# Optimization experiments

Hardware: AMD Instinct MI355X
Metric: run time of the kernel (lower is better)

## Reference

```python
import jax, jax.numpy as jnp
import numpy as np

# module constants (from init_kwargs)
CS, NV, ED = 8, 4, 32          # codebook_size, num_variables, embedding_dim
VIEWS, D, KSZ = 3, 16, 3        # num_input_channels, depth, kernel_size
HW = 14                         # 7 * scale (scale=2)
CSP = 8                         # spatial of conv_shape after three valid 3x3 convs: 14->12->10->8
KSTATES = CS ** NV              # 4096 combinatorial discrete states


def _elu(x):
    return jnp.where(x > 0, x, jnp.expm1(x))


def _conv_t(x, w, b):
    # PyTorch ConvTranspose2d(stride=1, padding=0); w: (Cin, Cout, k, k)
    wf = jnp.flip(w, (2, 3)).transpose(1, 0, 2, 3)  # -> (Cout, Cin, k, k)
    p = w.shape[2] - 1
    y = jax.lax.conv_general_dilated(x, wf, (1, 1), [(p, p), (p, p)],
                                     dimension_numbers=('NCHW', 'OIHW', 'NCHW'))
    return y + b[None, :, None, None]


def setup_inputs() -> dict:
    key = jax.random.key(0)
    ks = jax.random.split(key, 10)
    rn = lambda k, shape, s=1.0: jax.random.normal(k, shape, jnp.float32) * s
    return {
        'x': rn(ks[0], (64, VIEWS, HW, HW)),
        'latent_embedding': rn(ks[1], (NV, CS, ED)),
        'lin_w': rn(ks[2], (VIEWS, ED * NV, 4 * D * CSP * CSP), 0.05),
        'lin_b': rn(ks[3], (VIEWS, 4 * D * CSP * CSP), 0.05),
        'w1': rn(ks[4], (VIEWS, 4 * D, 2 * D, KSZ, KSZ), 0.05),
        'b1': rn(ks[5], (VIEWS, 2 * D), 0.05),
        'w2': rn(ks[6], (VIEWS, 2 * D, D, KSZ, KSZ), 0.05),
        'b2': rn(ks[7], (VIEWS, D), 0.05),
        'w3': rn(ks[8], (VIEWS, D, 1, KSZ, KSZ), 0.05),
        'b3': rn(ks[9], (VIEWS, 1), 0.05),
    }


def reference(x, latent_embedding, lin_w, lin_b, w1, b1, w2, b2, w3, b3):
    # all combinations of codebook indices (itertools.product order): [K, NV]
    all_idcs = jnp.stack(
        jnp.meshgrid(*([jnp.arange(CS)] * NV), indexing='ij'), -1).reshape(-1, NV)
    # gather: z[k, v, :] = latent_embedding[v, all_idcs[k, v], :]
    z = latent_embedding[jnp.arange(NV)[None, :], all_idcs]       # [K, NV, ED]
    zf = z.reshape(KSTATES, NV * ED)                              # 'b n d -> b (n d)'

    def decode(lw, lb, W1, B1, W2, B2, W3, B3):
        h = (zf @ lw + lb).reshape(KSTATES, 4 * D, CSP, CSP)
        h = _elu(_conv_t(h, W1, B1))
        h = _elu(_conv_t(h, W2, B2))
        h = _conv_t(h, W3, B3)
        return h[:, 0]                                            # [K, HW, HW]

    m = jax.vmap(decode)(lin_w, lin_b, w1, b1, w2, b2, w3, b3)    # [views, K, HW, HW]
    m = jnp.transpose(m, (1, 0, 2, 3))                            # [K, views, HW, HW]

    # obs_logits = -0.5 * sum_{h,w} (m[None] - x[:, None])**2, computed without
    # materializing the [B, K, views, HW, HW] broadcast tensor
    m2 = jnp.sum(m * m, axis=(-2, -1))                            # [K, views]
    x2 = jnp.sum(x * x, axis=(-2, -1))                            # [B, views]
    cross = jnp.einsum('kvhw,bvhw->bkv', m, x)                    # [B, K, views]
    return -0.5 * (m2[None] + x2[:, None] - 2.0 * cross)          # [B, K, views]
```

## Files before the change

### kernel.cpp

```cpp
#include <hip/hip_runtime.h>
#include <cstddef>


typedef __attribute__((ext_vector_type(4))) float f32x4;
typedef _Float16 half8v __attribute__((ext_vector_type(8)));
typedef _Float16 half4v __attribute__((ext_vector_type(4)));
typedef _Float16 half2v __attribute__((ext_vector_type(2)));

static __device__ __forceinline__ float elu(float s) {
    float e = __expf(s) - 1.0f;
    return s > 0.f ? s : e;
}
static __device__ __forceinline__ float dot2acc(int hpair, int wpair, float acc) {
#if __has_builtin(__builtin_amdgcn_fdot2)
    return __builtin_amdgcn_fdot2(__builtin_bit_cast(half2v, hpair),
                                  __builtin_bit_cast(half2v, wpair), acc, false);
#else
    half2v h = __builtin_bit_cast(half2v, hpair);
    half2v w = __builtin_bit_cast(half2v, wpair);
    acc = fmaf((float)h.x, (float)w.x, acc);
    return fmaf((float)h.y, (float)w.y, acc);
#endif
}
static __device__ __forceinline__ int sh2addr(int c, int r) {
    return c * 392 + r * 24 + (((r >> 2) & 3) << 3);
}

__global__ __launch_bounds__(320) void prep_kernel(const float* __restrict__ x,
                                                   const float* __restrict__ le,
                                                   const float* __restrict__ lin_w,
                                                   const float* __restrict__ lin_b,
                                                   const float* __restrict__ w1,
                                                   const float* __restrict__ b1,
                                                   const float* __restrict__ w2,
                                                   float* __restrict__ Qa,
                                                   float* __restrict__ Qb,
                                                   float* __restrict__ x2,
                                                   short* __restrict__ xB,
                                                   short* __restrict__ Wf) {
    int bid = blockIdx.x;
    int t = threadIdx.x;
    if (bid >= 198) {
        int pid = bid - 198;
        int v = pid % 3, part = pid / 3;
        if (part < 4) {
            int nb = part;
            short* xBv = xB + v * 14336 + nb * 3584;
            for (int idx = t; idx < 3584; idx += 320) {
                int j = idx & 7, lane = (idx >> 3) & 63, s = idx >> 9;
                int px = s * 32 + ((lane >> 4) << 3) + j;
                int b  = nb * 16 + (lane & 15);
                float val = (px < 196) ? x[(b * 3 + v) * 196 + px] : 0.f;
                _Float16 h = (_Float16)val;
                xBv[idx] = __builtin_bit_cast(short, h);
            }
        } else if (part == 4) {
            int w = t >> 6, lane = t & 63;
            for (int b = w; b < 64; b += 5) {
                const float* xp = x + (b * 3 + v) * 196;
                float s = 0.f;
                for (int px = lane; px < 196; px += 64) s = fmaf(xp[px], xp[px], s);
#pragma unroll
                for (int off = 32; off; off >>= 1) s += __shfl_down(s, off, 64);
                if (lane == 0) x2[v * 64 + b] = s;
            }
        } else if (t < 64) {
            int lane = t;
            const float* w2v = w2 + v * 32 * 16 * 9;
            int co = lane & 15;
            int cibase = (lane >> 4) * 8;
#pragma unroll
            for (int tap = 0; tap < 9; ++tap)
#pragma unroll
                for (int j = 0; j < 8; ++j) {
                    _Float16 h = (_Float16)w2v[((cibase + j) * 16 + co) * 9 + tap];
                    Wf[(((v * 9 + tap) * 64 + lane) << 3) + j] = __builtin_bit_cast(short, h);
                }
        }
        return;
    }
    __shared__ float sPt[64 * 144];
    __shared__ float sW[16 * 32 * 9];
    int row = bid % 33;
    int v   = (bid / 33) % 3;
    int z   = bid / 99;

    float pj[16];
    if (t < 256) {
        if (row < 32) {
            int vp = row >> 3;
            const float* base0 = lin_w + (size_t)v * 524288 + (size_t)vp * 131072 + t * 16;
            const float* lep = le + row * 32;
            f32x4 a0 = {0,0,0,0}, a1 = {0,0,0,0}, a2 = {0,0,0,0}, a3 = {0,0,0,0};
            for (int e = 0; e < 32; ++e) {
                float lv = lep[e];
                const float4* bp = (const float4*)(base0 + e * 4096);
                float4 b0 = bp[0], b1v_ = bp[1], b2v_ = bp[2], b3v_ = bp[3];
                a0[0] = fmaf(lv, b0.x, a0[0]);  a0[1] = fmaf(lv, b0.y, a0[1]);
                a0[2] = fmaf(lv, b0.z, a0[2]);  a0[3] = fmaf(lv, b0.w, a0[3]);
                a1[0] = fmaf(lv, b1v_.x, a1[0]); a1[1] = fmaf(lv, b1v_.y, a1[1]);
                a1[2] = fmaf(lv, b1v_.z, a1[2]); a1[3] = fmaf(lv, b1v_.w, a1[3]);
                a2[0] = fmaf(lv, b2v_.x, a2[0]); a2[1] = fmaf(lv, b2v_.y, a2[1]);
                a2[2] = fmaf(lv, b2v_.z, a2[2]); a2[3] = fmaf(lv, b2v_.w, a2[3]);
                a3[0] = fmaf(lv, b3v_.x, a3[0]); a3[1] = fmaf(lv, b3v_.y, a3[1]);
                a3[2] = fmaf(lv, b3v_.z, a3[2]); a3[3] = fmaf(lv, b3v_.w, a3[3]);
            }
#pragma unroll
            for (int j = 0; j < 4; ++j) {
                pj[j] = a0[j]; pj[4 + j] = a1[j]; pj[8 + j] = a2[j]; pj[12 + j] = a3[j];
            }
        } else {
            const float4* bp = (const float4*)(lin_b + v * 4096 + t * 16);
#pragma unroll
            for (int j = 0; j < 4; ++j) {
                float4 b = bp[j];
                pj[4 * j] = b.x; pj[4 * j + 1] = b.y; pj[4 * j + 2] = b.z; pj[4 * j + 3] = b.w;
            }
        }
    }
    float4* zp = (float4*)sPt;
    for (int i = t; i < 2304; i += 320) zp[i] = float4{0.f, 0.f, 0.f, 0.f};
    __syncthreads();
    if (t < 256) {
        int ci = t >> 2;
#pragma unroll
        for (int j = 0; j < 16; ++j) {
            int r = (t & 3) * 16 + j;
            int y = r >> 3, xx = r & 7;
            sPt[ci * 144 + (xx + 2) * 12 + (y + 2)] = pj[j];
        }
    }
    const float* w1v = w1 + (size_t)v * 18432;
    int co = t / 10, ox = t % 10;
    float acc[10];
#pragma unroll
    for (int i = 0; i < 10; ++i) acc[i] = 0.f;

    for (int c0 = z * 2; c0 < z * 2 + 2; ++c0) {
        __syncthreads();
        const float4* wsrc = (const float4*)(w1v + c0 * 4608);
        for (int i = t; i < 1152; i += 320) ((float4*)sW)[i] = wsrc[i];
        __syncthreads();
#pragma unroll 2
        for (int ci = 0; ci < 16; ++ci) {
            const float* xp = sPt + (c0 * 16 + ci) * 144;
            const float* wp = sW + (ci * 32 + co) * 9;
            float wv[9];
#pragma unroll
            for (int j = 0; j < 9; ++j) wv[j] = wp[j];
#pragma unroll
            for (int b = 0; b < 3; ++b) {
                const float* colp = xp + (ox + 2 - b) * 12;
                float4 c0v = *(const float4*)(colp);
                float4 c1v = *(const float4*)(colp + 4);
                float4 c2v = *(const float4*)(colp + 8);
                float cv[12] = {c0v.x, c0v.y, c0v.z, c0v.w,
                                c1v.x, c1v.y, c1v.z, c1v.w,
                                c2v.x, c2v.y, c2v.z, c2v.w};
#pragma unroll
                for (int a = 0; a < 3; ++a) {
                    float wgt = wv[a * 3 + b];
#pragma unroll
                    for (int oy = 0; oy < 10; ++oy)
                        acc[oy] = fmaf(cv[oy + 2 - a], wgt, acc[oy]);
                }
            }
        }
    }
    float bb = (z == 0 && row == 32) ? b1[v * 32 + co] : 0.f;
    float* dst = (z == 0 ? Qa : Qb) + (size_t)v * 105600 + row * 3200;
#pragma unroll
    for (int oy = 0; oy < 10; ++oy)
        dst[(ox * 10 + oy) * 32 + co] = acc[oy] + bb;
}

__global__ __launch_bounds__(256) void fusedgemm_kernel(const float* __restrict__ Qa,
                                                        const float* __restrict__ Qb,
                                                        const short* __restrict__ Wf,
                                                        const float* __restrict__ b2,
                                                        const float* __restrict__ w3,
                                                        const float* __restrict__ b3,
                                                        const short* __restrict__ xB,
                                                        const float* __restrict__ x2g,
                                                        float* __restrict__ out) {
    __shared__ alignas(16) short sH1[196 * 40];
    __shared__ alignas(16) short sH2[6280];
    __shared__ alignas(16) short sM[16 * 224];
    __shared__ alignas(16) float sQ[3200];
    __shared__ int sW3p[72];
    __shared__ float sM2[16];
    int k0 = blockIdx.x * 16;
    int v = blockIdx.y;
    int t = threadIdx.x;
    int lane = t & 63;
    int g = lane >> 4;
    int w = t >> 6;

    half8v bfrag[9];
#pragma unroll
    for (int tap = 0; tap < 9; ++tap)
        bfrag[tap] = *(const half8v*)(const void*)(Wf + (((v * 9 + tap) * 64 + lane) << 3));
    float bias2 = b2[v * 16 + (lane & 15)];
    float bias3 = b3[v];

    if (t < 16) sM2[t] = 0.f;
    for (int pix = t; pix < 196; pix += 256) {
        int c = pix / 14, r = pix % 14;
        if (c < 2 || c >= 12 || r < 2 || r >= 12) {
            int4* z = (int4*)(sH1 + pix * 40);
            z[0] = int4{0,0,0,0}; z[1] = int4{0,0,0,0};
            z[2] = int4{0,0,0,0}; z[3] = int4{0,0,0,0};
        }
    }
    {
        int c = t >> 4, r = t & 15;
        if (c < 2 || c >= 14 || r < 2 || r >= 14) {
            int4* z = (int4*)(sH2 + sh2addr(c, r));
            z[0] = int4{0,0,0,0}; z[1] = int4{0,0,0,0};
        }
    }
    if (t < 72) {
        int tap = t / 8, j = t % 8;
        half2v p = {(_Float16)w3[v * 144 + (2 * j) * 9 + tap],
                    (_Float16)w3[v * 144 + (2 * j + 1) * 9 + tap]};
        sW3p[t] = __builtin_bit_cast(int, p);
    }

    int st1[4]; bool v1[4];
    {
        int ci4 = (t & 7) * 4;
#pragma unroll
        for (int j = 0; j < 4; ++j) {
            int i = t + j * 256;
            v1[j] = (i < 800);
            int pix = i >> 3;
            int cx = pix / 10, ry = pix % 10;
            st1[j] = ((cx + 2) * 14 + (ry + 2)) * 40 + ci4;
        }
    }
    int ntile = 0; int bmoff[3]; int soff[3][4];
    for (int tile = w; tile < 9; tile += 4) {
        int m = tile * 16 + (lane & 15);
        int cx2 = m / 12, ry2 = m % 12;
        bmoff[ntile] = (cx2 * 14 + ry2) * 40 + g * 8;
        int p0 = tile * 16 + g * 4;
        int cxp = p0 / 12, ryp = p0 % 12;
        int co = lane & 15;
#pragma unroll
        for (int r = 0; r < 4; ++r) {
            soff[ntile][r] = sh2addr(cxp + 2, ryp + 2) + co;
            ++ryp; if (ryp == 12) { ryp = 0; ++cxp; }
        }
        ++ntile;
    }
    int off3[9];
    {
        int ry3 = (t < 196) ? t / 14 : 0;
        int cx3 = (t < 196) ? t % 14 : 0;
#pragma unroll
        for (int a = 0; a < 3; ++a)
#pragma unroll
            for (int b = 0; b < 3; ++b)
                off3[a * 3 + b] = sh2addr(cx3 + 2 - b, ry3 + 2 - a);
    }

    const float* Qav = Qa + (size_t)v * 105600;
    const float* Qbv = Qb + (size_t)v * 105600;
    int i0 = (k0 >> 9) & 7;
    int i1 = (k0 >> 6) & 7;
    int i2b = (k0 >> 3) & 7;

    for (int s = 0; s < 16; ++s) {
        if ((s & 7) == 0) {
            int i2 = i2b + (s >> 3);
            const float4* pa0 = (const float4*)(Qav + i0 * 3200);
            const float4* pb0 = (const float4*)(Qbv + i0 * 3200);
            const float4* pa1 = (const float4*)(Qav + (8 + i1) * 3200);
            const float4* pb1 = (const float4*)(Qbv + (8 + i1) * 3200);
            const float4* pa2 = (const float4*)(Qav + (16 + i2) * 3200);
            const float4* pb2 = (const float4*)(Qbv + (16 + i2) * 3200);
            const float4* pab = (const float4*)(Qav + 32 * 3200);
            const float4* pbb = (const float4*)(Qbv + 32 * 3200);
            float4* dq = (float4*)sQ;
            for (int i = t; i < 800; i += 256) {
                float4 A = pa0[i], B = pb0[i], C = pa1[i], D = pb1[i];
                float4 E = pa2[i], F = pb2[i], G = pab[i], H = pbb[i];
                dq[i] = float4{A.x + B.x + C.x + D.x + E.x + F.x + G.x + H.x,
                               A.y + B.y + C.y + D.y + E.y + F.y + G.y + H.y,
                               A.z + B.z + C.z + D.z + E.z + F.z + G.z + H.z,
                               A.w + B.w + C.w + D.w + E.w + F.w + G.w + H.w};
            }
            __syncthreads();
        }
        {
            int i3 = s & 7;
            const float4* qa3 = (const float4*)(Qav + (24 + i3) * 3200);
            const float4* qb3 = (const float4*)(Qbv + (24 + i3) * 3200);
            const float4* qs = (const float4*)sQ;
#pragma unroll
            for (int j = 0; j < 4; ++j) {
                if (v1[j]) {
                    int i = t + j * 256;
                    float4 q = qs[i], a = qa3[i], b = qb3[i];
                    half4v o = {(_Float16)elu(q.x + a.x + b.x),
                                (_Float16)elu(q.y + a.y + b.y),
                                (_Float16)elu(q.z + a.z + b.z),
                                (_Float16)elu(q.w + a.w + b.w)};
                    *(half4v*)(void*)(sH1 + st1[j]) = o;
                }
            }
        }
        __syncthreads();
#pragma unroll
        for (int it = 0; it < 3; ++it) {
            if (it < ntile) {
                const short* basemin = sH1 + bmoff[it];
                f32x4 acc0 = {bias2, bias2, bias2, bias2};
                f32x4 acc1 = {0.f, 0.f, 0.f, 0.f};
#pragma unroll
                for (int a = 0; a < 3; ++a)
#pragma unroll
                    for (int b = 0; b < 3; ++b) {
                        half8v af = *(const half8v*)(const void*)(basemin + ((2 - b) * 14 + (2 - a)) * 40);
                        int idx = a * 3 + b;
                        if (idx & 1)
                            acc1 = __builtin_amdgcn_mfma_f32_16x16x32_f16(af, bfrag[idx], acc1, 0, 0, 0);
                        else
                            acc0 = __builtin_amdgcn_mfma_f32_16x16x32_f16(af, bfrag[idx], acc0, 0, 0, 0);
                    }
#pragma unroll
                for (int r = 0; r < 4; ++r) {
                    _Float16 h = (_Float16)elu(acc0[r] + acc1[r]);
                    sH2[soff[it][r]] = __builtin_bit_cast(short, h);
                }
            }
        }
        __syncthreads();
        {
            float mval = 0.f;
            if (t < 196) {
                float a0 = bias3, a1 = 0.f, a2 = 0.f, a3 = 0.f;
#pragma unroll
                for (int tap = 0; tap < 9; ++tap) {
                    const short* base = sH2 + off3[tap];
                    int4 lo = *(const int4*)(const void*)(base);
                    int4 hi = *(const int4*)(const void*)(base + 8);
                    const int* wp = sW3p + tap * 8;
                    a0 = dot2acc(lo.x, wp[0], a0);
                    a1 = dot2acc(lo.y, wp[1], a1);
                    a2 = dot2acc(lo.z, wp[2], a2);
                    a3 = dot2acc(lo.w, wp[3], a3);
                    a0 = dot2acc(hi.x, wp[4], a0);
                    a1 = dot2acc(hi.y, wp[5], a1);
                    a2 = dot2acc(hi.z, wp[6], a2);
                    a3 = dot2acc(hi.w, wp[7], a3);
                }
                mval = (a0 + a1) + (a2 + a3);
            }
            if (t < 224) {
                _Float16 h = (_Float16)mval;
                sM[s * 224 + t] = __builtin_bit_cast(short, h);
            }
            float sq = mval * mval;
#pragma unroll
            for (int off = 32; off; off >>= 1) sq += __shfl_down(sq, off, 64);
            if (lane == 0) atomicAdd(&sM2[s], sq);
        }
    }
    __syncthreads();

    {
        f32x4 acc = {0.f, 0.f, 0.f, 0.f};
        const short* abase = sM + (lane & 15) * 224 + g * 8;
        const short* bbase = xB + (((v * 4 + w) * 7) * 64 + lane) * 8;
#pragma unroll
        for (int s7 = 0; s7 < 7; ++s7) {
            half8v af = *(const half8v*)(const void*)(abase + s7 * 32);
            half8v bf = *(const half8v*)(const void*)(bbase + s7 * 512);
            acc = __builtin_amdgcn_mfma_f32_16x16x32_f16(af, bf, acc, 0, 0, 0);
        }
        int b = w * 16 + (lane & 15);
        float x2v = x2g[v * 64 + b];
        size_t obase = ((size_t)b * 4096 + k0) * 3 + v;
#pragma unroll
        for (int r = 0; r < 4; ++r) {
            int kk = g * 4 + r;
            out[obase + (size_t)kk * 3] = acc[r] - 0.5f * (sM2[kk] + x2v);
        }
    }
}

extern "C" void kernel_launch(void* const* d_in, const int* in_sizes, int n_in,
                              void* d_out, int out_size, void* d_ws, size_t ws_size,
                              hipStream_t stream) {
    const float* x     = (const float*)d_in[0];
    const float* le    = (const float*)d_in[1];
    const float* lin_w = (const float*)d_in[2];
    const float* lin_b = (const float*)d_in[3];
    const float* w1    = (const float*)d_in[4];
    const float* b1    = (const float*)d_in[5];
    const float* w2    = (const float*)d_in[6];
    const float* b2    = (const float*)d_in[7];
    const float* w3    = (const float*)d_in[8];
    const float* b3    = (const float*)d_in[9];
    float* out = (float*)d_out;

    float* ws = (float*)d_ws;
    float* x2g  = ws;
    short* xB   = (short*)(ws + 192);
    short* Wf   = (short*)(ws + 21760);
    float* Qa   = ws + 28736;
    float* Qb   = ws + 345536;

    prep_kernel<<<216, 320, 0, stream>>>(x, le, lin_w, lin_b, w1, b1, w2,
                                         Qa, Qb, x2g, xB, Wf);
    fusedgemm_kernel<<<dim3(256, 3), 256, 0, stream>>>(Qa, Qb, Wf, b2, w3, b3,
                                                       xB, x2g, out);
}
```

Before: 173.8 us.

## Split the linear projection into its own kernel to remove redundant recomputation

```diff
diff --git a/kernel.cpp b/kernel.cpp
--- a/kernel.cpp
+++ b/kernel.cpp
@@ -26,10 +26,36 @@
     return c * 392 + r * 24 + (((r >> 2) & 3) << 3);
 }
 
-__global__ __launch_bounds__(320) void prep_kernel(const float* __restrict__ x,
-                                                   const float* __restrict__ le,
+__global__ __launch_bounds__(256) void pmat_kernel(const float* __restrict__ le,
                                                    const float* __restrict__ lin_w,
                                                    const float* __restrict__ lin_b,
+                                                   float* __restrict__ P3) {
+    int o = blockIdx.x * 256 + threadIdx.x;
+    int y = blockIdx.y;
+    int v = blockIdx.z;
+    if (y == 4) {
+        P3[((size_t)v * 33 + 32) * 4096 + o] = lin_b[v * 4096 + o];
+        return;
+    }
+    int vp = y;
+    const float* lwv = lin_w + (size_t)v * 524288 + (size_t)vp * 131072 + o;
+    float acc[8];
+#pragma unroll
+    for (int j = 0; j < 8; ++j) acc[j] = 0.f;
+    const float* lep = le + vp * 8 * 32;
+    for (int e = 0; e < 32; ++e) {
+        float lw = lwv[e * 4096];
+#pragma unroll
+        for (int j = 0; j < 8; ++j)
+            acc[j] = fmaf(lep[j * 32 + e], lw, acc[j]);
+    }
+#pragma unroll
+    for (int j = 0; j < 8; ++j)
+        P3[((size_t)v * 33 + vp * 8 + j) * 4096 + o] = acc[j];
+}
+
+__global__ __launch_bounds__(320) void prep_kernel(const float* __restrict__ x,
+                                                   const float* __restrict__ P3,
                                                    const float* __restrict__ w1,
                                                    const float* __restrict__ b1,
                                                    const float* __restrict__ w2,
@@ -79,56 +105,19 @@
         }
         return;
     }
-    __shared__ float sPt[64 * 144];
+    __shared__ float sPt[32 * 144];
     __shared__ float sW[16 * 32 * 9];
     int row = bid % 33;
     int v   = (bid / 33) % 3;
     int z   = bid / 99;
 
-    float pj[16];
-    if (t < 256) {
-        if (row < 32) {
-            int vp = row >> 3;
-            const float* base0 = lin_w + (size_t)v * 524288 + (size_t)vp * 131072 + t * 16;
-            const float* lep = le + row * 32;
-            f32x4 a0 = {0,0,0,0}, a1 = {0,0,0,0}, a2 = {0,0,0,0}, a3 = {0,0,0,0};
-            for (int e = 0; e < 32; ++e) {
-                float lv = lep[e];
-                const float4* bp = (const float4*)(base0 + e * 4096);
-                float4 b0 = bp[0], b1v_ = bp[1], b2v_ = bp[2], b3v_ = bp[3];
-                a0[0] = fmaf(lv, b0.x, a0[0]);  a0[1] = fmaf(lv, b0.y, a0[1]);
-                a0[2] = fmaf(lv, b0.z, a0[2]);  a0[3] = fmaf(lv, b0.w, a0[3]);
-                a1[0] = fmaf(lv, b1v_.x, a1[0]); a1[1] = fmaf(lv, b1v_.y, a1[1]);
-                a1[2] = fmaf(lv, b1v_.z, a1[2]); a1[3] = fmaf(lv, b1v_.w, a1[3]);
-                a2[0] = fmaf(lv, b2v_.x, a2[0]); a2[1] = fmaf(lv, b2v_.y, a2[1]);
-                a2[2] = fmaf(lv, b2v_.z, a2[2]); a2[3] = fmaf(lv, b2v_.w, a2[3]);
-                a3[0] = fmaf(lv, b3v_.x, a3[0]); a3[1] = fmaf(lv, b3v_.y, a3[1]);
-                a3[2] = fmaf(lv, b3v_.z, a3[2]); a3[3] = fmaf(lv, b3v_.w, a3[3]);
-            }
-#pragma unroll
-            for (int j = 0; j < 4; ++j) {
-                pj[j] = a0[j]; pj[4 + j] = a1[j]; pj[8 + j] = a2[j]; pj[12 + j] = a3[j];
-            }
-        } else {
-            const float4* bp = (const float4*)(lin_b + v * 4096 + t * 16);
-#pragma unroll
-            for (int j = 0; j < 4; ++j) {
-                float4 b = bp[j];
-                pj[4 * j] = b.x; pj[4 * j + 1] = b.y; pj[4 * j + 2] = b.z; pj[4 * j + 3] = b.w;
-            }
-        }
-    }
+    const float* src = P3 + ((size_t)v * 33 + row) * 4096 + z * 2048;
     float4* zp = (float4*)sPt;
-    for (int i = t; i < 2304; i += 320) zp[i] = float4{0.f, 0.f, 0.f, 0.f};
+    for (int i = t; i < 1152; i += 320) zp[i] = float4{0.f, 0.f, 0.f, 0.f};
     __syncthreads();
-    if (t < 256) {
-        int ci = t >> 2;
-#pragma unroll
-        for (int j = 0; j < 16; ++j) {
-            int r = (t & 3) * 16 + j;
-            int y = r >> 3, xx = r & 7;
-            sPt[ci * 144 + (xx + 2) * 12 + (y + 2)] = pj[j];
-        }
+    for (int i = t; i < 2048; i += 320) {
+        int ci = i >> 6, r = i & 63, y = r >> 3, xx = r & 7;
+        sPt[ci * 144 + (xx + 2) * 12 + (y + 2)] = src[i];
     }
     const float* w1v = w1 + (size_t)v * 18432;
     int co = t / 10, ox = t % 10;
@@ -136,14 +125,15 @@
 #pragma unroll
     for (int i = 0; i < 10; ++i) acc[i] = 0.f;
 
-    for (int c0 = z * 2; c0 < z * 2 + 2; ++c0) {
+    for (int c0l = 0; c0l < 2; ++c0l) {
+        int c0 = z * 2 + c0l;
         __syncthreads();
         const float4* wsrc = (const float4*)(w1v + c0 * 4608);
         for (int i = t; i < 1152; i += 320) ((float4*)sW)[i] = wsrc[i];
         __syncthreads();
 #pragma unroll 2
         for (int ci = 0; ci < 16; ++ci) {
-            const float* xp = sPt + (c0 * 16 + ci) * 144;
+            const float* xp = sPt + (c0l * 16 + ci) * 144;
             const float* wp = sW + (ci * 32 + co) * 9;
             float wv[9];
 #pragma unroll
@@ -411,9 +401,10 @@
     short* Wf   = (short*)(ws + 21760);
     float* Qa   = ws + 28736;
     float* Qb   = ws + 345536;
-
-    prep_kernel<<<216, 320, 0, stream>>>(x, le, lin_w, lin_b, w1, b1, w2,
-                                         Qa, Qb, x2g, xB, Wf);
+    float* P3   = ws + 662336;
+
+    pmat_kernel<<<dim3(16, 5, 3), 256, 0, stream>>>(le, lin_w, lin_b, P3);
+    prep_kernel<<<216, 320, 0, stream>>>(x, P3, w1, b1, w2, Qa, Qb, x2g, xB, Wf);
     fusedgemm_kernel<<<dim3(256, 3), 256, 0, stream>>>(Qa, Qb, Wf, b2, w3, b3,
                                                        xB, x2g, out);
 }
```

Measured after the change: 171.2 us. Within noise of the previous version (-1.5%).
